# Performance work log

Measured on AMD Instinct MI355X. Metric: run time of the kernel, lower is better.

The kernel has to match this reference:

```python
import jax, jax.numpy as jnp
import numpy as np

N, T, D, H = 8, 1024, 128, 8

def setup_inputs() -> dict:
    key = jax.random.key(0)
    ks = jax.random.split(key, 6)
    x = jax.random.normal(ks[0], (N, T, D), dtype=jnp.float32)
    attention_mask = jax.random.randint(ks[1], (N, 1, 1, T), 0, 2).astype(jnp.bool_)
    attention_weights = jax.random.uniform(ks[2], (N, H, T, T), dtype=jnp.float32)
    # Linear(dim -> heads*dim) weights, torch convention: W @ x^T + b, W: [H*D, D]
    s = 1.0 / np.sqrt(D)
    Wq = jax.random.normal(ks[3], (H * D, D), dtype=jnp.float32) * s
    Wk = jax.random.normal(ks[4], (H * D, D), dtype=jnp.float32) * s
    Wv = jax.random.normal(ks[5], (H * D, D), dtype=jnp.float32) * s
    bq = jnp.zeros((H * D,), jnp.float32)
    bk = jnp.zeros((H * D,), jnp.float32)
    bv = jnp.zeros((H * D,), jnp.float32)
    return {"x": x, "attention_mask": attention_mask, "attention_weights": attention_weights,
            "Wq": Wq, "bq": bq, "Wk": Wk, "bk": bk, "Wv": Wv, "bv": bv}

def reference(x, attention_mask, attention_weights, Wq, bq, Wk, bk, Wv, bv):
    n, t, d = x.shape
    h = Wq.shape[0] // d
    # projections: [N,T,H*D] -> [N,H,T,D]
    q = (x @ Wq.T + bq).reshape(n, t, h, d).transpose(0, 2, 1, 3)
    k = (x @ Wk.T + bk).reshape(n, t, h, d).transpose(0, 2, 1, 3)
    v = (x @ Wv.T + bv).reshape(n, t, h, d).transpose(0, 2, 1, 3)
    # scores [N,H,T,T]
    att = jnp.einsum('nhtd,nhsd->nhts', q, k) / np.sqrt(d).astype(np.float32)
    att = att * attention_weights
    att = jnp.where(attention_mask, -jnp.inf, att)
    att = jax.nn.softmax(att, axis=-1)
    out = jnp.einsum('nhts,nhsd->nhtd', att, v)
    out = out.transpose(0, 2, 1, 3).reshape(n, t, h * d)
    out_agg = jnp.mean(out, axis=1)
    return out, jax.lax.stop_gradient(out_agg), jax.lax.stop_gradient(att)
```

## Files before the change

### kernel.cpp

```cpp
#include <hip/hip_runtime.h>
#include <hip/hip_bf16.h>
#include <hip/hip_fp16.h>

#define NB 8
#define TT 1024
#define DD 128
#define HH 8

using short8  = __attribute__((ext_vector_type(8))) short;
using floatx4 = __attribute__((ext_vector_type(4))) float;
using half8   = __attribute__((ext_vector_type(8))) _Float16;
using half4   = __attribute__((ext_vector_type(4))) _Float16;
using intx4   = __attribute__((ext_vector_type(4))) int;

__device__ __forceinline__ unsigned short f2bf_u(float f) {
    union { float f; unsigned u; } v; v.f = f;
    return (unsigned short)((v.u + 0x7fffu + ((v.u >> 16) & 1u)) >> 16);
}

__global__ __launch_bounds__(256, 2) void proj_kernel(
    const float* __restrict__ x,
    const float* __restrict__ Wq, const float* __restrict__ bq,
    const float* __restrict__ Wk, const float* __restrict__ bk,
    const float* __restrict__ Wv, const float* __restrict__ bv,
    unsigned short* __restrict__ qb, unsigned short* __restrict__ kb,
    unsigned short* __restrict__ vt)
{
    int b     = blockIdx.x;
    int which = b >> 10;
    int rem   = b & 1023;
    int mblk  = rem >> 3;
    int nblk  = rem & 7;
    int tid   = threadIdx.x;
    int wid   = tid >> 6, lane = tid & 63;
    int l15   = lane & 15, quad = lane >> 4;
    int m0    = mblk * 64 + wid * 16;

    const float* W    = (which == 0) ? Wq : (which == 1) ? Wk : Wv;
    const float* bias = (which == 0) ? bq : (which == 1) ? bk : bv;
    unsigned short* dst = (which == 0) ? qb : (which == 1) ? kb : vt;

    short8 a[4];
    const float* xr = x + (size_t)(m0 + l15) * DD + quad * 8;
    #pragma unroll
    for (int kk = 0; kk < 4; ++kk) {
        const float* p = xr + kk * 32;
        short8 t;
        #pragma unroll
        for (int j = 0; j < 8; ++j) t[j] = (short)f2bf_u(p[j]);
        a[kk] = t;
    }

    floatx4 acc[8];
    #pragma unroll
    for (int ct = 0; ct < 8; ++ct) acc[ct] = (floatx4){0.f, 0.f, 0.f, 0.f};

    for (int ct = 0; ct < 8; ++ct) {
        int c = nblk * 128 + ct * 16 + l15;
        const float* wr = W + (size_t)c * DD + quad * 8;
        #pragma unroll
        for (int kk = 0; kk < 4; ++kk) {
            const float* p = wr + kk * 32;
            short8 bf;
            #pragma unroll
            for (int j = 0; j < 8; ++j) bf[j] = (short)f2bf_u(p[j]);
            acc[ct] = __builtin_amdgcn_mfma_f32_16x16x32_bf16(a[kk], bf, acc[ct], 0, 0, 0);
        }
    }

    #pragma unroll
    for (int ct = 0; ct < 8; ++ct) {
        int c  = nblk * 128 + ct * 16 + l15;
        int h  = c >> 7, dd = c & 127;
        float bsv = bias[c];
        #pragma unroll
        for (int r = 0; r < 4; ++r) {
            int m = m0 + quad * 4 + r;
            int n = m >> 10, t = m & 1023;
            unsigned short v = f2bf_u(acc[ct][r] + bsv);
            size_t idx;
            if (which == 2) idx = ((size_t)(n * HH + h) * DD + dd) * TT + t;
            else            idx = ((size_t)(n * HH + h) * TT + t) * DD + dd;
            dst[idx] = v;
        }
    }
}

#define SSTRIDE 1032

__global__ __launch_bounds__(256, 2) void attn_kernel(
    const unsigned short* __restrict__ qb, const unsigned short* __restrict__ kb,
    const unsigned short* __restrict__ vt,
    const float* __restrict__ wts, const int* __restrict__ mask,
    float* __restrict__ out, float* __restrict__ outagg, float* __restrict__ att)
{
    extern __shared__ char smem[];
    _Float16* S   = (_Float16*)smem;
    float* rowinv = (float*)(smem + 32 * SSTRIDE * 2);

    int b    = blockIdx.x;
    int slot = b & 7, j = b >> 3;
    int tile = j & 31, gq = j >> 5;
    int g    = gq * 8 + slot;
    int n    = g >> 3, h = g & 7;
    int t0   = tile * 32;

    int tid = threadIdx.x;
    int wid = tid >> 6, lane = tid & 63;
    int l15 = lane & 15, quad = lane >> 4;

    const unsigned short* qp = qb + ((size_t)g * TT + t0) * DD;
    const unsigned short* kp = kb + (size_t)g * TT * DD;
    const unsigned short* vp = vt + (size_t)g * DD * TT;
    const float* wp = wts + (size_t)g * TT * TT + (size_t)t0 * TT;
    const int*   mp = mask + n * TT;
    float* attp = att + (size_t)g * TT * TT + (size_t)t0 * TT;

    short8 aq[2][4];
    #pragma unroll
    for (int rt = 0; rt < 2; ++rt)
        #pragma unroll
        for (int kk = 0; kk < 4; ++kk)
            aq[rt][kk] = *(const short8*)(qp + (size_t)(rt * 16 + l15) * DD + kk * 32 + quad * 8);

    const int c0 = wid * 256;
    const float scale = 0.08838834764831845f;

    const float* wrow0 = wp + (size_t)l15 * TT + c0 + quad * 4;
    const float* wrow1 = wrow0 + (size_t)16 * TT;
    const unsigned short* kcol = kp + (size_t)(c0 + l15) * DD + quad * 8;
    const int* mrow = mp + c0 + quad * 4;
    _Float16* sst0 = S + (size_t)l15 * SSTRIDE + c0 + quad * 4;
    _Float16* sst1 = sst0 + (size_t)16 * SSTRIDE;

    floatx4 w0_c, w1_c, w0_n, w1_n;
    intx4   mk_c, mk_n;
    short8  kf[4];

    w0_c = *(const floatx4*)(wrow0);
    w1_c = *(const floatx4*)(wrow1);
    mk_c = *(const intx4*)(mrow);
    w0_n = *(const floatx4*)(wrow0 + 16);
    w1_n = *(const floatx4*)(wrow1 + 16);
    mk_n = *(const intx4*)(mrow + 16);
    #pragma unroll
    for (int kk = 0; kk < 4; ++kk)
        kf[kk] = *(const short8*)(kcol + kk * 32);

    for (int ct = 0; ct < 16; ++ct) {
        int ctk = (ct + 1 < 16) ? ct + 1 : 15;
        int ctw = (ct + 2 < 16) ? ct + 2 : 15;
        short8 kn[4];
        #pragma unroll
        for (int kk = 0; kk < 4; ++kk)
            kn[kk] = *(const short8*)(kcol + ctk * 16 * DD + kk * 32);
        floatx4 nw0 = *(const floatx4*)(wrow0 + ctw * 16);
        floatx4 nw1 = *(const floatx4*)(wrow1 + ctw * 16);
        intx4   nmk = *(const intx4*)(mrow + ctw * 16);

        floatx4 acc0 = {0.f,0.f,0.f,0.f}, acc1 = {0.f,0.f,0.f,0.f};
        #pragma unroll
        for (int kk = 0; kk < 4; ++kk) {
            acc0 = __builtin_amdgcn_mfma_f32_16x16x32_bf16(kf[kk], aq[0][kk], acc0, 0, 0, 0);
            acc1 = __builtin_amdgcn_mfma_f32_16x16x32_bf16(kf[kk], aq[1][kk], acc1, 0, 0, 0);
        }

        half4 h0, h1;
        #pragma unroll
        for (int r = 0; r < 4; ++r) {
            h0[r] = (_Float16)(mk_c[r] ? -65504.f : acc0[r] * scale * w0_c[r]);
            h1[r] = (_Float16)(mk_c[r] ? -65504.f : acc1[r] * scale * w1_c[r]);
        }
        *(half4*)(sst0 + ct * 16) = h0;
        *(half4*)(sst1 + ct * 16) = h1;

        #pragma unroll
        for (int kk = 0; kk < 4; ++kk) kf[kk] = kn[kk];
        w0_c = w0_n; w1_c = w1_n; mk_c = mk_n;
        w0_n = nw0;  w1_n = nw1;  mk_n = nmk;
    }
    __syncthreads();

    int row = tid >> 3;
    int jj  = tid & 7;
    _Float16* Srow = S + row * SSTRIDE + jj * 8;

    half8 hv[16];
    #pragma unroll
    for (int i = 0; i < 16; ++i) hv[i] = *(const half8*)(Srow + i * 64);

    float m8[8];
    #pragma unroll
    for (int e = 0; e < 8; ++e) m8[e] = (float)hv[0][e];
    #pragma unroll
    for (int i = 1; i < 16; ++i)
        #pragma unroll
        for (int e = 0; e < 8; ++e) m8[e] = fmaxf(m8[e], (float)hv[i][e]);
    float mx = fmaxf(fmaxf(fmaxf(m8[0], m8[1]), fmaxf(m8[2], m8[3])),
                     fmaxf(fmaxf(m8[4], m8[5]), fmaxf(m8[6], m8[7])));
    mx = fmaxf(mx, __shfl_xor(mx, 1));
    mx = fmaxf(mx, __shfl_xor(mx, 2));
    mx = fmaxf(mx, __shfl_xor(mx, 4));

    float s8[8] = {0.f,0.f,0.f,0.f,0.f,0.f,0.f,0.f};
    #pragma unroll
    for (int i = 0; i < 16; ++i)
        #pragma unroll
        for (int e = 0; e < 8; ++e) s8[e] += __expf((float)hv[i][e] - mx);
    float sum = ((s8[0] + s8[1]) + (s8[2] + s8[3])) + ((s8[4] + s8[5]) + (s8[6] + s8[7]));
    sum += __shfl_xor(sum, 1);
    sum += __shfl_xor(sum, 2);
    sum += __shfl_xor(sum, 4);
    float iv = 1.f / sum;
    if (jj == 0) rowinv[row] = iv;

    float* arow = attp + (size_t)row * TT + jj * 8;
    #pragma unroll
    for (int i = 0; i < 16; ++i) {
        half8 ev;
        floatx4 o0, o1;
        #pragma unroll
        for (int e = 0; e < 8; ++e) {
            float ex = __expf((float)hv[i][e] - mx);
            ev[e] = __builtin_bit_cast(_Float16, f2bf_u(ex));
            float a = ex * iv;
            if (e < 4) o0[e] = a; else o1[e - 4] = a;
        }
        *(half8*)(Srow + i * 64) = ev;
        __builtin_nontemporal_store(o0, (floatx4*)(arow + i * 64));
        __builtin_nontemporal_store(o1, (floatx4*)(arow + i * 64 + 4));
    }
    __syncthreads();

    int c0p = wid * 32;
    const unsigned short* vrow0 = vp + (size_t)(c0p + l15) * TT + quad * 8;
    const unsigned short* vrow1 = vp + (size_t)(c0p + 16 + l15) * TT + quad * 8;
    const _Float16* sp0 = S + (size_t)l15 * SSTRIDE + quad * 8;
    const _Float16* sp1 = S + (size_t)(16 + l15) * SSTRIDE + quad * 8;

    floatx4 o00 = {0.f,0.f,0.f,0.f}, o01 = o00, o10 = o00, o11 = o00;
    short8 vb0 = *(const short8*)(vrow0);
    short8 vb1 = *(const short8*)(vrow1);
    short8 pa0 = __builtin_bit_cast(short8, *(const half8*)(sp0));
    short8 pa1 = __builtin_bit_cast(short8, *(const half8*)(sp1));

    for (int ks = 0; ks < 32; ++ks) {
        int ksn = (ks + 1 < 32) ? ks + 1 : 31;
        short8 nv0 = *(const short8*)(vrow0 + ksn * 32);
        short8 nv1 = *(const short8*)(vrow1 + ksn * 32);
        short8 na0 = __builtin_bit_cast(short8, *(const half8*)(sp0 + ksn * 32));
        short8 na1 = __builtin_bit_cast(short8, *(const half8*)(sp1 + ksn * 32));

        o00 = __builtin_amdgcn_mfma_f32_16x16x32_bf16(pa0, vb0, o00, 0, 0, 0);
        o01 = __builtin_amdgcn_mfma_f32_16x16x32_bf16(pa0, vb1, o01, 0, 0, 0);
        o10 = __builtin_amdgcn_mfma_f32_16x16x32_bf16(pa1, vb0, o10, 0, 0, 0);
        o11 = __builtin_amdgcn_mfma_f32_16x16x32_bf16(pa1, vb1, o11, 0, 0, 0);

        vb0 = nv0; vb1 = nv1; pa0 = na0; pa1 = na1;
    }

    #pragma unroll
    for (int ct = 0; ct < 2; ++ct) {
        int col = c0p + ct * 16 + l15;
        float agg = 0.f;
        #pragma unroll
        for (int rt = 0; rt < 2; ++rt) {
            floatx4 oo = (rt == 0) ? (ct == 0 ? o00 : o01) : (ct == 0 ? o10 : o11);
            #pragma unroll
            for (int r = 0; r < 4; ++r) {
                int rw = rt * 16 + quad * 4 + r;
                float val = oo[r] * rowinv[rw];
                __builtin_nontemporal_store(
                    val, &out[((size_t)(n * TT + t0 + rw)) * (HH * DD) + h * DD + col]);
                agg += val;
            }
        }
        atomicAdd(outagg + n * (HH * DD) + h * DD + col, agg * (1.f / (float)TT));
    }
}

extern "C" void kernel_launch(void* const* d_in, const int* in_sizes, int n_in,
                              void* d_out, int out_size, void* d_ws, size_t ws_size,
                              hipStream_t stream) {
    const float* x    = (const float*)d_in[0];
    const int*   mask = (const int*)d_in[1];
    const float* wts  = (const float*)d_in[2];
    const float* Wq = (const float*)d_in[3];
    const float* bq = (const float*)d_in[4];
    const float* Wk = (const float*)d_in[5];
    const float* bk = (const float*)d_in[6];
    const float* Wv = (const float*)d_in[7];
    const float* bv = (const float*)d_in[8];

    float* out    = (float*)d_out;
    float* outagg = out + (size_t)NB * TT * HH * DD;
    float* att    = outagg + NB * HH * DD;

    unsigned short* qb = (unsigned short*)d_ws;
    unsigned short* kb = qb + (size_t)NB * HH * TT * DD;
    unsigned short* vt = kb + (size_t)NB * HH * TT * DD;

    hipMemsetAsync(outagg, 0, (size_t)NB * HH * DD * sizeof(float), stream);
    proj_kernel<<<3072, 256, 0, stream>>>(x, Wq, bq, Wk, bk, Wv, bv, qb, kb, vt);
    attn_kernel<<<2048, 256, 32 * SSTRIDE * 2 + 128, stream>>>(
        qb, kb, vt, wts, mask, out, outagg, att);
}
```

Baseline: 738.0 us.

## Halve attention query tile to 16 rows and raise occupancy to 4 blocks

Shrinks each attention block from 32 to 16 query rows, doubling the grid and halving LDS use so launch bounds can target 4 blocks per CU. The weights/mask prefetch becomes a 4-deep ring buffer, and the PV loop is fully unrolled with 2-deep prefetch. The attention and output stores switch from nontemporal to ordinary stores. In exchange, every K and V tile is now read twice as often across blocks, and there are twice as many atomic adds into the aggregate output.

```diff
diff --git a/kernel.cpp b/kernel.cpp
--- a/kernel.cpp
+++ b/kernel.cpp
@@ -87,8 +87,9 @@
 }
 
 #define SSTRIDE 1032
-
-__global__ __launch_bounds__(256, 2) void attn_kernel(
+#define QROWS 16
+
+__global__ __launch_bounds__(256, 4) void attn_kernel(
     const unsigned short* __restrict__ qb, const unsigned short* __restrict__ kb,
     const unsigned short* __restrict__ vt,
     const float* __restrict__ wts, const int* __restrict__ mask,
@@ -96,14 +97,14 @@
 {
     extern __shared__ char smem[];
     _Float16* S   = (_Float16*)smem;
-    float* rowinv = (float*)(smem + 32 * SSTRIDE * 2);
+    float* rowinv = (float*)(smem + QROWS * SSTRIDE * 2);
 
     int b    = blockIdx.x;
     int slot = b & 7, j = b >> 3;
-    int tile = j & 31, gq = j >> 5;
+    int tile = j & 63, gq = j >> 6;
     int g    = gq * 8 + slot;
     int n    = g >> 3, h = g & 7;
-    int t0   = tile * 32;
+    int t0   = tile * QROWS;
 
     int tid = threadIdx.x;
     int wid = tid >> 6, lane = tid & 63;
@@ -116,84 +117,73 @@
     const int*   mp = mask + n * TT;
     float* attp = att + (size_t)g * TT * TT + (size_t)t0 * TT;
 
-    short8 aq[2][4];
-    #pragma unroll
-    for (int rt = 0; rt < 2; ++rt)
-        #pragma unroll
-        for (int kk = 0; kk < 4; ++kk)
-            aq[rt][kk] = *(const short8*)(qp + (size_t)(rt * 16 + l15) * DD + kk * 32 + quad * 8);
+    short8 aq[4];
+    #pragma unroll
+    for (int kk = 0; kk < 4; ++kk)
+        aq[kk] = *(const short8*)(qp + (size_t)l15 * DD + kk * 32 + quad * 8);
 
     const int c0 = wid * 256;
     const float scale = 0.08838834764831845f;
 
-    const float* wrow0 = wp + (size_t)l15 * TT + c0 + quad * 4;
-    const float* wrow1 = wrow0 + (size_t)16 * TT;
+    const float* wrow = wp + (size_t)l15 * TT + c0 + quad * 4;
     const unsigned short* kcol = kp + (size_t)(c0 + l15) * DD + quad * 8;
     const int* mrow = mp + c0 + quad * 4;
-    _Float16* sst0 = S + (size_t)l15 * SSTRIDE + c0 + quad * 4;
-    _Float16* sst1 = sst0 + (size_t)16 * SSTRIDE;
-
-    floatx4 w0_c, w1_c, w0_n, w1_n;
-    intx4   mk_c, mk_n;
-    short8  kf[4];
-
-    w0_c = *(const floatx4*)(wrow0);
-    w1_c = *(const floatx4*)(wrow1);
-    mk_c = *(const intx4*)(mrow);
-    w0_n = *(const floatx4*)(wrow0 + 16);
-    w1_n = *(const floatx4*)(wrow1 + 16);
-    mk_n = *(const intx4*)(mrow + 16);
-    #pragma unroll
-    for (int kk = 0; kk < 4; ++kk)
-        kf[kk] = *(const short8*)(kcol + kk * 32);
-
+    _Float16* sst = S + (size_t)l15 * SSTRIDE + c0 + quad * 4;
+
+    floatx4 wbuf[4]; intx4 mbuf[4];
+    #pragma unroll
+    for (int p = 0; p < 4; ++p) {
+        wbuf[p] = *(const floatx4*)(wrow + p * 16);
+        mbuf[p] = *(const intx4*)(mrow + p * 16);
+    }
+    short8 kf[4];
+    #pragma unroll
+    for (int kk = 0; kk < 4; ++kk) kf[kk] = *(const short8*)(kcol + kk * 32);
+
+    #pragma unroll
     for (int ct = 0; ct < 16; ++ct) {
-        int ctk = (ct + 1 < 16) ? ct + 1 : 15;
-        int ctw = (ct + 2 < 16) ? ct + 2 : 15;
+        const int ctk = (ct + 1 < 16) ? ct + 1 : 15;
         short8 kn[4];
         #pragma unroll
         for (int kk = 0; kk < 4; ++kk)
             kn[kk] = *(const short8*)(kcol + ctk * 16 * DD + kk * 32);
-        floatx4 nw0 = *(const floatx4*)(wrow0 + ctw * 16);
-        floatx4 nw1 = *(const floatx4*)(wrow1 + ctw * 16);
-        intx4   nmk = *(const intx4*)(mrow + ctw * 16);
-
-        floatx4 acc0 = {0.f,0.f,0.f,0.f}, acc1 = {0.f,0.f,0.f,0.f};
-        #pragma unroll
-        for (int kk = 0; kk < 4; ++kk) {
-            acc0 = __builtin_amdgcn_mfma_f32_16x16x32_bf16(kf[kk], aq[0][kk], acc0, 0, 0, 0);
-            acc1 = __builtin_amdgcn_mfma_f32_16x16x32_bf16(kf[kk], aq[1][kk], acc1, 0, 0, 0);
-        }
-
-        half4 h0, h1;
-        #pragma unroll
-        for (int r = 0; r < 4; ++r) {
-            h0[r] = (_Float16)(mk_c[r] ? -65504.f : acc0[r] * scale * w0_c[r]);
-            h1[r] = (_Float16)(mk_c[r] ? -65504.f : acc1[r] * scale * w1_c[r]);
-        }
-        *(half4*)(sst0 + ct * 16) = h0;
-        *(half4*)(sst1 + ct * 16) = h1;
+        floatx4 nw; intx4 nmk;
+        if (ct + 4 < 16) {
+            nw  = *(const floatx4*)(wrow + (ct + 4) * 16);
+            nmk = *(const intx4*)(mrow + (ct + 4) * 16);
+        }
+
+        floatx4 acc = {0.f, 0.f, 0.f, 0.f};
+        #pragma unroll
+        for (int kk = 0; kk < 4; ++kk)
+            acc = __builtin_amdgcn_mfma_f32_16x16x32_bf16(kf[kk], aq[kk], acc, 0, 0, 0);
+
+        floatx4 w = wbuf[ct & 3]; intx4 mk = mbuf[ct & 3];
+        half4 hh;
+        #pragma unroll
+        for (int r = 0; r < 4; ++r)
+            hh[r] = (_Float16)(mk[r] ? -65504.f : acc[r] * scale * w[r]);
+        *(half4*)(sst + ct * 16) = hh;
 
         #pragma unroll
         for (int kk = 0; kk < 4; ++kk) kf[kk] = kn[kk];
-        w0_c = w0_n; w1_c = w1_n; mk_c = mk_n;
-        w0_n = nw0;  w1_n = nw1;  mk_n = nmk;
+        if (ct + 4 < 16) { wbuf[ct & 3] = nw; mbuf[ct & 3] = nmk; }
     }
     __syncthreads();
 
-    int row = tid >> 3;
-    int jj  = tid & 7;
+    int row = tid >> 4;
+    int jj  = tid & 15;
     _Float16* Srow = S + row * SSTRIDE + jj * 8;
 
-    half8 hv[16];
-    #pragma unroll
-    for (int i = 0; i < 16; ++i) hv[i] = *(const half8*)(Srow + i * 64);
+    half8 hv[8];
+    #pragma unroll
+    for (int i = 0; i < 8; ++i) hv[i] = *(const half8*)(Srow + i * 128);
 
     float m8[8];
     #pragma unroll
     for (int e = 0; e < 8; ++e) m8[e] = (float)hv[0][e];
     #pragma unroll
-    for (int i = 1; i < 16; ++i)
+    for (int i = 1; i < 8; ++i)
         #pragma unroll
         for (int e = 0; e < 8; ++e) m8[e] = fmaxf(m8[e], (float)hv[i][e]);
     float mx = fmaxf(fmaxf(fmaxf(m8[0], m8[1]), fmaxf(m8[2], m8[3])),
@@ -201,22 +191,24 @@
     mx = fmaxf(mx, __shfl_xor(mx, 1));
     mx = fmaxf(mx, __shfl_xor(mx, 2));
     mx = fmaxf(mx, __shfl_xor(mx, 4));
+    mx = fmaxf(mx, __shfl_xor(mx, 8));
 
     float s8[8] = {0.f,0.f,0.f,0.f,0.f,0.f,0.f,0.f};
     #pragma unroll
-    for (int i = 0; i < 16; ++i)
+    for (int i = 0; i < 8; ++i)
         #pragma unroll
         for (int e = 0; e < 8; ++e) s8[e] += __expf((float)hv[i][e] - mx);
     float sum = ((s8[0] + s8[1]) + (s8[2] + s8[3])) + ((s8[4] + s8[5]) + (s8[6] + s8[7]));
     sum += __shfl_xor(sum, 1);
     sum += __shfl_xor(sum, 2);
     sum += __shfl_xor(sum, 4);
+    sum += __shfl_xor(sum, 8);
     float iv = 1.f / sum;
     if (jj == 0) rowinv[row] = iv;
 
     float* arow = attp + (size_t)row * TT + jj * 8;
     #pragma unroll
-    for (int i = 0; i < 16; ++i) {
+    for (int i = 0; i < 8; ++i) {
         half8 ev;
         floatx4 o0, o1;
         #pragma unroll
@@ -226,54 +218,49 @@
             float a = ex * iv;
             if (e < 4) o0[e] = a; else o1[e - 4] = a;
         }
-        *(half8*)(Srow + i * 64) = ev;
-        __builtin_nontemporal_store(o0, (floatx4*)(arow + i * 64));
-        __builtin_nontemporal_store(o1, (floatx4*)(arow + i * 64 + 4));
+        *(half8*)(Srow + i * 128) = ev;
+        *(floatx4*)(arow + i * 128)     = o0;
+        *(floatx4*)(arow + i * 128 + 4) = o1;
     }
     __syncthreads();
 
     int c0p = wid * 32;
     const unsigned short* vrow0 = vp + (size_t)(c0p + l15) * TT + quad * 8;
     const unsigned short* vrow1 = vp + (size_t)(c0p + 16 + l15) * TT + quad * 8;
-    const _Float16* sp0 = S + (size_t)l15 * SSTRIDE + quad * 8;
-    const _Float16* sp1 = S + (size_t)(16 + l15) * SSTRIDE + quad * 8;
-
-    floatx4 o00 = {0.f,0.f,0.f,0.f}, o01 = o00, o10 = o00, o11 = o00;
-    short8 vb0 = *(const short8*)(vrow0);
-    short8 vb1 = *(const short8*)(vrow1);
-    short8 pa0 = __builtin_bit_cast(short8, *(const half8*)(sp0));
-    short8 pa1 = __builtin_bit_cast(short8, *(const half8*)(sp1));
-
+    const _Float16* sp = S + (size_t)l15 * SSTRIDE + quad * 8;
+
+    floatx4 o0 = {0.f,0.f,0.f,0.f}, o1 = o0;
+    short8 vb0[2], vb1[2], pa[2];
+    #pragma unroll
+    for (int p = 0; p < 2; ++p) {
+        vb0[p] = *(const short8*)(vrow0 + p * 32);
+        vb1[p] = *(const short8*)(vrow1 + p * 32);
+        pa[p]  = __builtin_bit_cast(short8, *(const half8*)(sp + p * 32));
+    }
+    #pragma unroll
     for (int ks = 0; ks < 32; ++ks) {
-        int ksn = (ks + 1 < 32) ? ks + 1 : 31;
-        short8 nv0 = *(const short8*)(vrow0 + ksn * 32);
-        short8 nv1 = *(const short8*)(vrow1 + ksn * 32);
-        short8 na0 = __builtin_bit_cast(short8, *(const half8*)(sp0 + ksn * 32));
-        short8 na1 = __builtin_bit_cast(short8, *(const half8*)(sp1 + ksn * 32));
-
-        o00 = __builtin_amdgcn_mfma_f32_16x16x32_bf16(pa0, vb0, o00, 0, 0, 0);
-        o01 = __builtin_amdgcn_mfma_f32_16x16x32_bf16(pa0, vb1, o01, 0, 0, 0);
-        o10 = __builtin_amdgcn_mfma_f32_16x16x32_bf16(pa1, vb0, o10, 0, 0, 0);
-        o11 = __builtin_amdgcn_mfma_f32_16x16x32_bf16(pa1, vb1, o11, 0, 0, 0);
-
-        vb0 = nv0; vb1 = nv1; pa0 = na0; pa1 = na1;
+        const int sl = ks & 1;
+        short8 a = pa[sl], b0 = vb0[sl], b1 = vb1[sl];
+        if (ks + 2 < 32) {
+            vb0[sl] = *(const short8*)(vrow0 + (ks + 2) * 32);
+            vb1[sl] = *(const short8*)(vrow1 + (ks + 2) * 32);
+            pa[sl]  = __builtin_bit_cast(short8, *(const half8*)(sp + (ks + 2) * 32));
+        }
+        o0 = __builtin_amdgcn_mfma_f32_16x16x32_bf16(a, b0, o0, 0, 0, 0);
+        o1 = __builtin_amdgcn_mfma_f32_16x16x32_bf16(a, b1, o1, 0, 0, 0);
     }
 
     #pragma unroll
     for (int ct = 0; ct < 2; ++ct) {
         int col = c0p + ct * 16 + l15;
+        floatx4 oo = (ct == 0) ? o0 : o1;
         float agg = 0.f;
         #pragma unroll
-        for (int rt = 0; rt < 2; ++rt) {
-            floatx4 oo = (rt == 0) ? (ct == 0 ? o00 : o01) : (ct == 0 ? o10 : o11);
-            #pragma unroll
-            for (int r = 0; r < 4; ++r) {
-                int rw = rt * 16 + quad * 4 + r;
-                float val = oo[r] * rowinv[rw];
-                __builtin_nontemporal_store(
-                    val, &out[((size_t)(n * TT + t0 + rw)) * (HH * DD) + h * DD + col]);
-                agg += val;
-            }
+        for (int r = 0; r < 4; ++r) {
+            int rw = quad * 4 + r;
+            float val = oo[r] * rowinv[rw];
+            out[((size_t)(n * TT + t0 + rw)) * (HH * DD) + h * DD + col] = val;
+            agg += val;
         }
         atomicAdd(outagg + n * (HH * DD) + h * DD + col, agg * (1.f / (float)TT));
     }
@@ -302,6 +289,6 @@
 
     hipMemsetAsync(outagg, 0, (size_t)NB * HH * DD * sizeof(float), stream);
     proj_kernel<<<3072, 256, 0, stream>>>(x, Wq, bq, Wk, bk, Wv, bv, qb, kb, vt);
-    attn_kernel<<<2048, 256, 32 * SSTRIDE * 2 + 128, stream>>>(
+    attn_kernel<<<4096, 256, QROWS * SSTRIDE * 2 + 64, stream>>>(
         qb, kb, vt, wts, mask, out, outagg, att);
 }
```

After: 868.7 us. 1.18x slower.

## Deepen load prefetch to a 3-stage ring and hoist V loads before softmax writes

Applied to the files above, without the earlier changes.

Replaces the one-ahead register double-buffering in the QK^T and PV loops with 4-slot register rings that prefetch three iterations ahead, fully unrolling both loops. The first V tiles are issued before the softmax output write loop so their latency overlaps the attention-matrix stores. Nontemporal stores for the attention matrix and output are also replaced with ordinary stores. The deeper prefetch raises register pressure under the 2-waves launch bound and may cause spills, and plain stores can pollute cache for the large attention output.

```diff
diff --git a/kernel.cpp b/kernel.cpp
--- a/kernel.cpp
+++ b/kernel.cpp
@@ -133,51 +133,50 @@
     _Float16* sst0 = S + (size_t)l15 * SSTRIDE + c0 + quad * 4;
     _Float16* sst1 = sst0 + (size_t)16 * SSTRIDE;
 
-    floatx4 w0_c, w1_c, w0_n, w1_n;
-    intx4   mk_c, mk_n;
-    short8  kf[4];
-
-    w0_c = *(const floatx4*)(wrow0);
-    w1_c = *(const floatx4*)(wrow1);
-    mk_c = *(const intx4*)(mrow);
-    w0_n = *(const floatx4*)(wrow0 + 16);
-    w1_n = *(const floatx4*)(wrow1 + 16);
-    mk_n = *(const intx4*)(mrow + 16);
-    #pragma unroll
-    for (int kk = 0; kk < 4; ++kk)
-        kf[kk] = *(const short8*)(kcol + kk * 32);
-
+    short8  kring[4][4];
+    floatx4 wring[4][2];
+    intx4   mring[4];
+
+    #pragma unroll
+    for (int p = 0; p < 3; ++p) {
+        #pragma unroll
+        for (int kk = 0; kk < 4; ++kk)
+            kring[p][kk] = *(const short8*)(kcol + p * 16 * DD + kk * 32);
+        wring[p][0] = *(const floatx4*)(wrow0 + p * 16);
+        wring[p][1] = *(const floatx4*)(wrow1 + p * 16);
+        mring[p]    = *(const intx4*)(mrow + p * 16);
+    }
+
+    #pragma unroll
     for (int ct = 0; ct < 16; ++ct) {
-        int ctk = (ct + 1 < 16) ? ct + 1 : 15;
-        int ctw = (ct + 2 < 16) ? ct + 2 : 15;
-        short8 kn[4];
-        #pragma unroll
-        for (int kk = 0; kk < 4; ++kk)
-            kn[kk] = *(const short8*)(kcol + ctk * 16 * DD + kk * 32);
-        floatx4 nw0 = *(const floatx4*)(wrow0 + ctw * 16);
-        floatx4 nw1 = *(const floatx4*)(wrow1 + ctw * 16);
-        intx4   nmk = *(const intx4*)(mrow + ctw * 16);
+        if (ct + 3 < 16) {
+            const int pf = ct + 3, sp = pf & 3;
+            #pragma unroll
+            for (int kk = 0; kk < 4; ++kk)
+                kring[sp][kk] = *(const short8*)(kcol + pf * 16 * DD + kk * 32);
+            wring[sp][0] = *(const floatx4*)(wrow0 + pf * 16);
+            wring[sp][1] = *(const floatx4*)(wrow1 + pf * 16);
+            mring[sp]    = *(const intx4*)(mrow + pf * 16);
+        }
+        const int sl = ct & 3;
 
         floatx4 acc0 = {0.f,0.f,0.f,0.f}, acc1 = {0.f,0.f,0.f,0.f};
         #pragma unroll
         for (int kk = 0; kk < 4; ++kk) {
-            acc0 = __builtin_amdgcn_mfma_f32_16x16x32_bf16(kf[kk], aq[0][kk], acc0, 0, 0, 0);
-            acc1 = __builtin_amdgcn_mfma_f32_16x16x32_bf16(kf[kk], aq[1][kk], acc1, 0, 0, 0);
-        }
-
+            acc0 = __builtin_amdgcn_mfma_f32_16x16x32_bf16(kring[sl][kk], aq[0][kk], acc0, 0, 0, 0);
+            acc1 = __builtin_amdgcn_mfma_f32_16x16x32_bf16(kring[sl][kk], aq[1][kk], acc1, 0, 0, 0);
+        }
+
+        floatx4 w0 = wring[sl][0], w1 = wring[sl][1];
+        intx4 mk = mring[sl];
         half4 h0, h1;
         #pragma unroll
         for (int r = 0; r < 4; ++r) {
-            h0[r] = (_Float16)(mk_c[r] ? -65504.f : acc0[r] * scale * w0_c[r]);
-            h1[r] = (_Float16)(mk_c[r] ? -65504.f : acc1[r] * scale * w1_c[r]);
+            h0[r] = (_Float16)(mk[r] ? -65504.f : acc0[r] * scale * w0[r]);
+            h1[r] = (_Float16)(mk[r] ? -65504.f : acc1[r] * scale * w1[r]);
         }
         *(half4*)(sst0 + ct * 16) = h0;
         *(half4*)(sst1 + ct * 16) = h1;
-
-        #pragma unroll
-        for (int kk = 0; kk < 4; ++kk) kf[kk] = kn[kk];
-        w0_c = w0_n; w1_c = w1_n; mk_c = mk_n;
-        w0_n = nw0;  w1_n = nw1;  mk_n = nmk;
     }
     __syncthreads();
 
@@ -214,6 +213,16 @@
     float iv = 1.f / sum;
     if (jj == 0) rowinv[row] = iv;
 
+    int c0p = wid * 32;
+    const unsigned short* vrow0 = vp + (size_t)(c0p + l15) * TT + quad * 8;
+    const unsigned short* vrow1 = vp + (size_t)(c0p + 16 + l15) * TT + quad * 8;
+    short8 vr0[4], vr1[4];
+    #pragma unroll
+    for (int p = 0; p < 3; ++p) {
+        vr0[p] = *(const short8*)(vrow0 + p * 32);
+        vr1[p] = *(const short8*)(vrow1 + p * 32);
+    }
+
     float* arow = attp + (size_t)row * TT + jj * 8;
     #pragma unroll
     for (int i = 0; i < 16; ++i) {
@@ -227,36 +236,36 @@
             if (e < 4) o0[e] = a; else o1[e - 4] = a;
         }
         *(half8*)(Srow + i * 64) = ev;
-        __builtin_nontemporal_store(o0, (floatx4*)(arow + i * 64));
-        __builtin_nontemporal_store(o1, (floatx4*)(arow + i * 64 + 4));
+        *(floatx4*)(arow + i * 64)     = o0;
+        *(floatx4*)(arow + i * 64 + 4) = o1;
     }
     __syncthreads();
 
-    int c0p = wid * 32;
-    const unsigned short* vrow0 = vp + (size_t)(c0p + l15) * TT + quad * 8;
-    const unsigned short* vrow1 = vp + (size_t)(c0p + 16 + l15) * TT + quad * 8;
     const _Float16* sp0 = S + (size_t)l15 * SSTRIDE + quad * 8;
     const _Float16* sp1 = S + (size_t)(16 + l15) * SSTRIDE + quad * 8;
 
+    short8 pr0[4], pr1[4];
+    #pragma unroll
+    for (int p = 0; p < 3; ++p) {
+        pr0[p] = __builtin_bit_cast(short8, *(const half8*)(sp0 + p * 32));
+        pr1[p] = __builtin_bit_cast(short8, *(const half8*)(sp1 + p * 32));
+    }
+
     floatx4 o00 = {0.f,0.f,0.f,0.f}, o01 = o00, o10 = o00, o11 = o00;
-    short8 vb0 = *(const short8*)(vrow0);
-    short8 vb1 = *(const short8*)(vrow1);
-    short8 pa0 = __builtin_bit_cast(short8, *(const half8*)(sp0));
-    short8 pa1 = __builtin_bit_cast(short8, *(const half8*)(sp1));
-
+    #pragma unroll
     for (int ks = 0; ks < 32; ++ks) {
-        int ksn = (ks + 1 < 32) ? ks + 1 : 31;
-        short8 nv0 = *(const short8*)(vrow0 + ksn * 32);
-        short8 nv1 = *(const short8*)(vrow1 + ksn * 32);
-        short8 na0 = __builtin_bit_cast(short8, *(const half8*)(sp0 + ksn * 32));
-        short8 na1 = __builtin_bit_cast(short8, *(const half8*)(sp1 + ksn * 32));
-
-        o00 = __builtin_amdgcn_mfma_f32_16x16x32_bf16(pa0, vb0, o00, 0, 0, 0);
-        o01 = __builtin_amdgcn_mfma_f32_16x16x32_bf16(pa0, vb1, o01, 0, 0, 0);
-        o10 = __builtin_amdgcn_mfma_f32_16x16x32_bf16(pa1, vb0, o10, 0, 0, 0);
-        o11 = __builtin_amdgcn_mfma_f32_16x16x32_bf16(pa1, vb1, o11, 0, 0, 0);
-
-        vb0 = nv0; vb1 = nv1; pa0 = na0; pa1 = na1;
+        if (ks + 3 < 32) {
+            const int pf = ks + 3, sp = pf & 3;
+            vr0[sp] = *(const short8*)(vrow0 + pf * 32);
+            vr1[sp] = *(const short8*)(vrow1 + pf * 32);
+            pr0[sp] = __builtin_bit_cast(short8, *(const half8*)(sp0 + pf * 32));
+            pr1[sp] = __builtin_bit_cast(short8, *(const half8*)(sp1 + pf * 32));
+        }
+        const int sl = ks & 3;
+        o00 = __builtin_amdgcn_mfma_f32_16x16x32_bf16(pr0[sl], vr0[sl], o00, 0, 0, 0);
+        o01 = __builtin_amdgcn_mfma_f32_16x16x32_bf16(pr0[sl], vr1[sl], o01, 0, 0, 0);
+        o10 = __builtin_amdgcn_mfma_f32_16x16x32_bf16(pr1[sl], vr0[sl], o10, 0, 0, 0);
+        o11 = __builtin_amdgcn_mfma_f32_16x16x32_bf16(pr1[sl], vr1[sl], o11, 0, 0, 0);
     }
 
     #pragma unroll
@@ -270,8 +279,7 @@
             for (int r = 0; r < 4; ++r) {
                 int rw = rt * 16 + quad * 4 + r;
                 float val = oo[r] * rowinv[rw];
-                __builtin_nontemporal_store(
-                    val, &out[((size_t)(n * TT + t0 + rw)) * (HH * DD) + h * DD + col]);
+                out[((size_t)(n * TT + t0 + rw)) * (HH * DD) + h * DD + col] = val;
                 agg += val;
             }
         }
```

Measured after the change: 788.1 us. 1.07x slower.
